# Kernel tuning notes

Measured on AMD Instinct MI355X. Metric: run time of the kernel, lower is better.

Reference implementation:

```python
import jax, jax.numpy as jnp
import numpy as np

LN_EPS = 1e-5  # torch LayerNorm default


def setup_inputs() -> dict:
    key = jax.random.key(0)
    k1, k2, k3 = jax.random.split(key, 3)
    B, L, D = 8, 2048, 1024
    CS, CD = 8192, 16
    x = jax.random.normal(k1, (B, L, D), dtype=jnp.float32)
    # xavier_uniform for Linear(dim, codebook_dim): bound = sqrt(6/(fan_in+fan_out))
    bound = float(np.sqrt(6.0 / (D + CD)))
    W = jax.random.uniform(k2, (CD, D), dtype=jnp.float32, minval=-bound, maxval=bound)
    codebook = jax.random.normal(k3, (CS, CD), dtype=jnp.float32)
    return {"x": x, "W": W, "codebook": codebook}


def reference(x, W, codebook):
    # random projection: (B,L,D) @ (D,CD) -> (B,L,CD)
    z = jnp.einsum("bld,cd->blc", x, W)
    # LayerNorm over last dim, no affine
    mu = jnp.mean(z, axis=-1, keepdims=True)
    var = jnp.mean(jnp.square(z - mu), axis=-1, keepdims=True)
    z = (z - mu) / jnp.sqrt(var + LN_EPS)
    # squared euclidean distance via matmul decomposition (avoids (B,L,CS,CD) tensor):
    # ||z - c||^2 = ||z||^2 - 2 z.c + ||c||^2 ; argmin is identical to argmin of the norm
    z_sq = jnp.sum(jnp.square(z), axis=-1, keepdims=True)        # (B,L,1)
    c_sq = jnp.sum(jnp.square(codebook), axis=-1)                # (CS,)
    d2 = z_sq - 2.0 * jnp.einsum("blc,kc->blk", z, codebook) + c_sq  # (B,L,CS)
    codes = jnp.argmin(d2, axis=-1)                              # (B,L) int32
    return codes
```

## Files before the change

kernel.cpp:

```cpp
#include <hip/hip_runtime.h>
#include <math.h>

#define D      1024
#define CD     16
#define CS     8192
#define ROWS   16384
#define LN_EPS 1e-5f
#define KCHUNK 512
#define NCHUNK (CS / KCHUNK)

typedef __attribute__((ext_vector_type(8))) short short8;
typedef __attribute__((ext_vector_type(4))) float f32x4;

__device__ inline unsigned short bf16_rne(float v) {
    unsigned u = __float_as_uint(v);
    unsigned r = u + 0x7FFFu + ((u >> 16) & 1u);
    return (unsigned short)(r >> 16);
}
__device__ inline short8 ld8(const unsigned short* p) { return *(const short8*)p; }

__device__ inline void split3(float v, unsigned short& a, unsigned short& b, unsigned short& c) {
    unsigned u = __float_as_uint(v);
    unsigned r = u + 0x7FFFu + ((u >> 16) & 1u);
    a = (unsigned short)(r >> 16);
    float r1 = v - __uint_as_float(r & 0xFFFF0000u);
    unsigned u1 = __float_as_uint(r1);
    unsigned r1b = u1 + 0x7FFFu + ((u1 >> 16) & 1u);
    b = (unsigned short)(r1b >> 16);
    float r2 = r1 - __uint_as_float(r1b & 0xFFFF0000u);
    c = bf16_rne(r2);
}

__global__ __launch_bounds__(256) void pack_all(const float* __restrict__ W,
                                                const float* __restrict__ cb,
                                                unsigned short* __restrict__ wb,
                                                unsigned short* __restrict__ cbp,
                                                float* __restrict__ nhc)
{
    const int t = threadIdx.x;
    if (blockIdx.x < 32) {
        int k = blockIdx.x * 256 + t;
        const float* c = cb + (long)k * CD;
        unsigned short* o = cbp + (long)k * 48;
        float csq = 0.f;
        #pragma unroll
        for (int d = 0; d < 16; ++d) {
            float v = c[d];
            csq = fmaf(v, v, csq);
            unsigned short h0, h1, h2;
            split3(v, h0, h1, h2);
            o[d] = h0; o[16 + d] = h1; o[32 + d] = h2;
        }
        nhc[k] = -0.5f * csq;
    } else {
        int tid = (blockIdx.x - 32) * 256 + t;
        int gk   = tid / 192;
        int rem  = tid % 192;
        int term = rem >> 6;
        int L    = rem & 63;
        int n = L & 15, q = L >> 4;
        const float* src = W + n * D + gk * 32 + q * 8;
        unsigned short* dst = wb + (size_t)tid * 8;
        #pragma unroll
        for (int j = 0; j < 8; ++j) {
            unsigned short h0, h1, h2;
            split3(src[j], h0, h1, h2);
            dst[j] = term == 0 ? h0 : (term == 1 ? h1 : h2);
        }
    }
}

__global__ __launch_bounds__(256, 4) void proj_ln(const float* __restrict__ x,
                                                  const unsigned short* __restrict__ wb,
                                                  unsigned short* __restrict__ zp)
{
    __shared__ float part[2][64][4];
    const int t = threadIdx.x;
    const int L = t & 63;
    const int w = t >> 6;
    const int tb = w & 1;
    const int kh = w >> 1;
    const int rt = blockIdx.x * 2 + tb;
    const int n = L & 15, q = L >> 4;

    const float* xrow = x + (size_t)(rt * 16 + n) * D + kh * 512 + q * 8;
    const unsigned short* wbase = wb + (size_t)(kh * 16) * 1536;

    f32x4 acc = {0.f, 0.f, 0.f, 0.f};
    #pragma unroll 4
    for (int kk = 0; kk < 16; ++kk) {
        float4 xa = *(const float4*)(xrow + kk * 32);
        float4 xb = *(const float4*)(xrow + kk * 32 + 4);
        const unsigned short* wp = wbase + (size_t)kk * 1536 + L * 8;
        short8 w0 = ld8(wp);
        short8 w1 = ld8(wp + 512);
        short8 w2 = ld8(wp + 1024);
        float vs[8] = {xa.x, xa.y, xa.z, xa.w, xb.x, xb.y, xb.z, xb.w};
        short8 x0, x1, x2;
        #pragma unroll
        for (int j = 0; j < 8; ++j) {
            unsigned short h0, h1, h2;
            split3(vs[j], h0, h1, h2);
            x0[j] = (short)h0; x1[j] = (short)h1; x2[j] = (short)h2;
        }
        acc = __builtin_amdgcn_mfma_f32_16x16x32_bf16(x0, w0, acc, 0, 0, 0);
        acc = __builtin_amdgcn_mfma_f32_16x16x32_bf16(x0, w1, acc, 0, 0, 0);
        acc = __builtin_amdgcn_mfma_f32_16x16x32_bf16(x1, w0, acc, 0, 0, 0);
        acc = __builtin_amdgcn_mfma_f32_16x16x32_bf16(x1, w1, acc, 0, 0, 0);
        acc = __builtin_amdgcn_mfma_f32_16x16x32_bf16(x0, w2, acc, 0, 0, 0);
        acc = __builtin_amdgcn_mfma_f32_16x16x32_bf16(x2, w0, acc, 0, 0, 0);
    }

    if (kh == 1) {
        #pragma unroll
        for (int r = 0; r < 4; ++r) part[tb][L][r] = acc[r];
    }
    __syncthreads();
    if (kh == 0) {
        #pragma unroll
        for (int r = 0; r < 4; ++r) {
            float zv = acc[r] + part[tb][L][r];
            float s = zv;
            for (int m = 1; m < 16; m <<= 1) s += __shfl_xor(s, m, 64);
            float mu = s * (1.f / 16.f);
            float dd = zv - mu;
            float v2 = dd * dd;
            for (int m = 1; m < 16; m <<= 1) v2 += __shfl_xor(v2, m, 64);
            float var = v2 * (1.f / 16.f);
            float zn = dd / sqrtf(var + LN_EPS);
            unsigned short h0, h1, h2;
            split3(zn, h0, h1, h2);
            unsigned short* zr = zp + (size_t)(rt * 16 + q * 4 + r) * 48;
            zr[n] = h0; zr[16 + n] = h1; zr[32 + n] = h2;
        }
    }
}

__global__ __launch_bounds__(512, 4) void dist_argmin(const unsigned short* __restrict__ zp,
                                                      const unsigned short* __restrict__ cbp,
                                                      const float* __restrict__ nhc,
                                                      float* __restrict__ pbest,
                                                      int* __restrict__ pidx)
{
    __shared__ __align__(16) unsigned short cl[KCHUNK * 48];
    __shared__ float ql[KCHUNK];
    const int t = threadIdx.x;
    const int kbase = blockIdx.y * KCHUNK;

    {
        float4* dst = (float4*)cl;
        const float4* src = (const float4*)(cbp + (size_t)kbase * 48);
        #pragma unroll
        for (int i = 0; i < 6; ++i) dst[t + i * 512] = src[t + i * 512];
        if (t < KCHUNK / 4) ((float4*)ql)[t] = ((const float4*)(nhc + kbase))[t];
    }
    __syncthreads();

    const int L = t & 63;
    const int w = t >> 6;
    const int n = L & 15;
    const int q = L >> 4;

    const int oa2 = (q * 8 + 16) & 31;
    const int oa3 = q < 2 ? 32 + q * 8 : (q - 2) * 8;
    const int ob3 = q < 2 ? q * 8 : 16 + q * 8;

    short8 a1[4], a2[4], a3[4];
    const int rt0 = blockIdx.x * 32 + w * 4;
    #pragma unroll
    for (int j = 0; j < 4; ++j) {
        const unsigned short* zr = zp + (size_t)((rt0 + j) * 16 + n) * 48;
        a1[j] = ld8(zr + q * 8);
        a2[j] = ld8(zr + oa2);
        a3[j] = ld8(zr + oa3);
    }

    float best[4][4];
    int   bi[4][4];
    #pragma unroll
    for (int j = 0; j < 4; ++j)
        #pragma unroll
        for (int r = 0; r < 4; ++r) { best[j][r] = -INFINITY; bi[j][r] = 0; }

    for (int tt = 0; tt < KCHUNK / 16; ++tt) {
        const unsigned short* cb_t = cl + (size_t)(tt * 16 + n) * 48;
        short8 b1 = ld8(cb_t + q * 8);
        short8 b3 = ld8(cb_t + ob3);
        float bneg = ql[tt * 16 + n];
        f32x4 bias = {bneg, bneg, bneg, bneg};
        int code = kbase + tt * 16 + n;
        f32x4 acc[4];
        #pragma unroll
        for (int j = 0; j < 4; ++j)
            acc[j] = __builtin_amdgcn_mfma_f32_16x16x32_bf16(a1[j], b1, bias, 0, 0, 0);
        #pragma unroll
        for (int j = 0; j < 4; ++j)
            acc[j] = __builtin_amdgcn_mfma_f32_16x16x32_bf16(a2[j], b1, acc[j], 0, 0, 0);
        #pragma unroll
        for (int j = 0; j < 4; ++j)
            acc[j] = __builtin_amdgcn_mfma_f32_16x16x32_bf16(a3[j], b3, acc[j], 0, 0, 0);
        #pragma unroll
        for (int j = 0; j < 4; ++j)
            #pragma unroll
            for (int r = 0; r < 4; ++r)
                if (acc[j][r] > best[j][r]) { best[j][r] = acc[j][r]; bi[j][r] = code; }
    }

    #pragma unroll
    for (int mask = 1; mask < 16; mask <<= 1) {
        #pragma unroll
        for (int j = 0; j < 4; ++j)
            #pragma unroll
            for (int r = 0; r < 4; ++r) {
                float s2 = __shfl_xor(best[j][r], mask, 64);
                int   i2 = __shfl_xor(bi[j][r], mask, 64);
                if (s2 > best[j][r] || (s2 == best[j][r] && i2 < bi[j][r])) {
                    best[j][r] = s2; bi[j][r] = i2;
                }
            }
    }
    if (n == 0) {
        #pragma unroll
        for (int j = 0; j < 4; ++j)
            #pragma unroll
            for (int r = 0; r < 4; ++r) {
                int row = (rt0 + j) * 16 + q * 4 + r;
                pbest[(size_t)row * NCHUNK + blockIdx.y] = best[j][r];
                pidx [(size_t)row * NCHUNK + blockIdx.y] = bi[j][r];
            }
    }
}

__global__ __launch_bounds__(256) void merge_argmin(const float* __restrict__ pbest,
                                                    const int* __restrict__ pidx,
                                                    int* __restrict__ out)
{
    const long row = (long)blockIdx.x * 256 + threadIdx.x;
    float best = -INFINITY;
    int   bi   = 0;
    #pragma unroll
    for (int i = 0; i < NCHUNK; ++i) {
        float s = pbest[row * NCHUNK + i];
        if (s > best) { best = s; bi = pidx[row * NCHUNK + i]; }
    }
    out[row] = bi;
}

extern "C" void kernel_launch(void* const* d_in, const int* in_sizes, int n_in,
                              void* d_out, int out_size, void* d_ws, size_t ws_size,
                              hipStream_t stream)
{
    const float* x  = (const float*)d_in[0];
    const float* W  = (const float*)d_in[1];
    const float* cb = (const float*)d_in[2];
    int* out = (int*)d_out;

    char* ws = (char*)d_ws;
    unsigned short* zp  = (unsigned short*)ws;
    unsigned short* cbp = (unsigned short*)(ws + 0x180000);
    float* nhc  = (float*)(ws + 0x240000);
    unsigned short* wb = (unsigned short*)(ws + 0x248000);
    float* pbest = (float*)(ws + 0x260000);
    int*   pidx  = (int*)  (ws + 0x360000);

    pack_all<<<56, 256, 0, stream>>>(W, cb, wb, cbp, nhc);
    proj_ln <<<ROWS / 32, 256, 0, stream>>>(x, wb, zp);
    dist_argmin<<<dim3(32, NCHUNK), 512, 0, stream>>>(zp, cbp, nhc, pbest, pidx);
    merge_argmin<<<ROWS / 256, 256, 0, stream>>>(pbest, pidx, out);
}
```

Baseline: 140.4 us.

## Split projection K across four waves and halve rows per wave in distance kernel

proj_ln now gives each block one 16-row tile and splits the 1024-wide reduction across four waves. Each wave keeps two independent MFMA accumulators to shorten the dependency chain, and the partial sums are reduced through shared memory. dist_argmin gives each wave two row tiles instead of four and launches twice as many blocks along x, with the inner code loop unrolled by two. Both changes aim for more parallelism and latency hiding. The cost is more codebook-chunk LDS loads per row, and the extra blocks redo that staging.

```diff
diff --git a/kernel.cpp b/kernel.cpp
--- a/kernel.cpp
+++ b/kernel.cpp
@@ -74,21 +74,20 @@
                                                   const unsigned short* __restrict__ wb,
                                                   unsigned short* __restrict__ zp)
 {
-    __shared__ float part[2][64][4];
+    __shared__ float part[3][64][4];
     const int t = threadIdx.x;
     const int L = t & 63;
-    const int w = t >> 6;
-    const int tb = w & 1;
-    const int kh = w >> 1;
-    const int rt = blockIdx.x * 2 + tb;
+    const int kq = t >> 6;
+    const int rt = blockIdx.x;
     const int n = L & 15, q = L >> 4;
 
-    const float* xrow = x + (size_t)(rt * 16 + n) * D + kh * 512 + q * 8;
-    const unsigned short* wbase = wb + (size_t)(kh * 16) * 1536;
-
-    f32x4 acc = {0.f, 0.f, 0.f, 0.f};
-    #pragma unroll 4
-    for (int kk = 0; kk < 16; ++kk) {
+    const float* xrow = x + (size_t)(rt * 16 + n) * D + kq * 256 + q * 8;
+    const unsigned short* wbase = wb + (size_t)(kq * 8) * 1536;
+
+    f32x4 acc0 = {0.f, 0.f, 0.f, 0.f};
+    f32x4 acc1 = {0.f, 0.f, 0.f, 0.f};
+    #pragma unroll
+    for (int kk = 0; kk < 8; ++kk) {
         float4 xa = *(const float4*)(xrow + kk * 32);
         float4 xb = *(const float4*)(xrow + kk * 32 + 4);
         const unsigned short* wp = wbase + (size_t)kk * 1536 + L * 8;
@@ -103,23 +102,23 @@
             split3(vs[j], h0, h1, h2);
             x0[j] = (short)h0; x1[j] = (short)h1; x2[j] = (short)h2;
         }
-        acc = __builtin_amdgcn_mfma_f32_16x16x32_bf16(x0, w0, acc, 0, 0, 0);
-        acc = __builtin_amdgcn_mfma_f32_16x16x32_bf16(x0, w1, acc, 0, 0, 0);
-        acc = __builtin_amdgcn_mfma_f32_16x16x32_bf16(x1, w0, acc, 0, 0, 0);
-        acc = __builtin_amdgcn_mfma_f32_16x16x32_bf16(x1, w1, acc, 0, 0, 0);
-        acc = __builtin_amdgcn_mfma_f32_16x16x32_bf16(x0, w2, acc, 0, 0, 0);
-        acc = __builtin_amdgcn_mfma_f32_16x16x32_bf16(x2, w0, acc, 0, 0, 0);
-    }
-
-    if (kh == 1) {
-        #pragma unroll
-        for (int r = 0; r < 4; ++r) part[tb][L][r] = acc[r];
+        acc0 = __builtin_amdgcn_mfma_f32_16x16x32_bf16(x0, w0, acc0, 0, 0, 0);
+        acc1 = __builtin_amdgcn_mfma_f32_16x16x32_bf16(x0, w1, acc1, 0, 0, 0);
+        acc0 = __builtin_amdgcn_mfma_f32_16x16x32_bf16(x1, w0, acc0, 0, 0, 0);
+        acc1 = __builtin_amdgcn_mfma_f32_16x16x32_bf16(x1, w1, acc1, 0, 0, 0);
+        acc0 = __builtin_amdgcn_mfma_f32_16x16x32_bf16(x0, w2, acc0, 0, 0, 0);
+        acc1 = __builtin_amdgcn_mfma_f32_16x16x32_bf16(x2, w0, acc1, 0, 0, 0);
+    }
+
+    if (kq != 0) {
+        #pragma unroll
+        for (int r = 0; r < 4; ++r) part[kq - 1][L][r] = acc0[r] + acc1[r];
     }
     __syncthreads();
-    if (kh == 0) {
+    if (kq == 0) {
         #pragma unroll
         for (int r = 0; r < 4; ++r) {
-            float zv = acc[r] + part[tb][L][r];
+            float zv = acc0[r] + acc1[r] + part[0][L][r] + part[1][L][r] + part[2][L][r];
             float s = zv;
             for (int m = 1; m < 16; m <<= 1) s += __shfl_xor(s, m, 64);
             float mu = s * (1.f / 16.f);
@@ -165,23 +164,24 @@
     const int oa3 = q < 2 ? 32 + q * 8 : (q - 2) * 8;
     const int ob3 = q < 2 ? q * 8 : 16 + q * 8;
 
-    short8 a1[4], a2[4], a3[4];
-    const int rt0 = blockIdx.x * 32 + w * 4;
-    #pragma unroll
-    for (int j = 0; j < 4; ++j) {
+    short8 a1[2], a2[2], a3[2];
+    const int rt0 = blockIdx.x * 16 + w * 2;
+    #pragma unroll
+    for (int j = 0; j < 2; ++j) {
         const unsigned short* zr = zp + (size_t)((rt0 + j) * 16 + n) * 48;
         a1[j] = ld8(zr + q * 8);
         a2[j] = ld8(zr + oa2);
         a3[j] = ld8(zr + oa3);
     }
 
-    float best[4][4];
-    int   bi[4][4];
-    #pragma unroll
-    for (int j = 0; j < 4; ++j)
+    float best[2][4];
+    int   bi[2][4];
+    #pragma unroll
+    for (int j = 0; j < 2; ++j)
         #pragma unroll
         for (int r = 0; r < 4; ++r) { best[j][r] = -INFINITY; bi[j][r] = 0; }
 
+    #pragma unroll 2
     for (int tt = 0; tt < KCHUNK / 16; ++tt) {
         const unsigned short* cb_t = cl + (size_t)(tt * 16 + n) * 48;
         short8 b1 = ld8(cb_t + q * 8);
@@ -189,18 +189,18 @@
         float bneg = ql[tt * 16 + n];
         f32x4 bias = {bneg, bneg, bneg, bneg};
         int code = kbase + tt * 16 + n;
-        f32x4 acc[4];
-        #pragma unroll
-        for (int j = 0; j < 4; ++j)
+        f32x4 acc[2];
+        #pragma unroll
+        for (int j = 0; j < 2; ++j)
             acc[j] = __builtin_amdgcn_mfma_f32_16x16x32_bf16(a1[j], b1, bias, 0, 0, 0);
         #pragma unroll
-        for (int j = 0; j < 4; ++j)
+        for (int j = 0; j < 2; ++j)
             acc[j] = __builtin_amdgcn_mfma_f32_16x16x32_bf16(a2[j], b1, acc[j], 0, 0, 0);
         #pragma unroll
-        for (int j = 0; j < 4; ++j)
+        for (int j = 0; j < 2; ++j)
             acc[j] = __builtin_amdgcn_mfma_f32_16x16x32_bf16(a3[j], b3, acc[j], 0, 0, 0);
         #pragma unroll
-        for (int j = 0; j < 4; ++j)
+        for (int j = 0; j < 2; ++j)
             #pragma unroll
             for (int r = 0; r < 4; ++r)
                 if (acc[j][r] > best[j][r]) { best[j][r] = acc[j][r]; bi[j][r] = code; }
@@ -209,7 +209,7 @@
     #pragma unroll
     for (int mask = 1; mask < 16; mask <<= 1) {
         #pragma unroll
-        for (int j = 0; j < 4; ++j)
+        for (int j = 0; j < 2; ++j)
             #pragma unroll
             for (int r = 0; r < 4; ++r) {
                 float s2 = __shfl_xor(best[j][r], mask, 64);
@@ -221,7 +221,7 @@
     }
     if (n == 0) {
         #pragma unroll
-        for (int j = 0; j < 4; ++j)
+        for (int j = 0; j < 2; ++j)
             #pragma unroll
             for (int r = 0; r < 4; ++r) {
                 int row = (rt0 + j) * 16 + q * 4 + r;
@@ -264,7 +264,7 @@
     int*   pidx  = (int*)  (ws + 0x360000);
 
     pack_all<<<56, 256, 0, stream>>>(W, cb, wb, cbp, nhc);
-    proj_ln <<<ROWS / 32, 256, 0, stream>>>(x, wb, zp);
-    dist_argmin<<<dim3(32, NCHUNK), 512, 0, stream>>>(zp, cbp, nhc, pbest, pidx);
+    proj_ln <<<ROWS / 16, 256, 0, stream>>>(x, wb, zp);
+    dist_argmin<<<dim3(ROWS / 256, NCHUNK), 512, 0, stream>>>(zp, cbp, nhc, pbest, pidx);
     merge_argmin<<<ROWS / 256, 256, 0, stream>>>(pbest, pidx, out);
 }
```

After: 139.1 us. No clear change (-0.9%).
